# Kernel optimization log

Hardware: AMD Instinct MI355X
Metric: run time of the kernel (lower is better)

## Reference

```python
import jax, jax.numpy as jnp
import numpy as np

N, E = 50000, 800000
D_IN, HID, HEADS, D_OUT = 128, 32, 4, 40
NEG_SLOPE = 0.2
BN_EPS = 1e-5


def gat_conv(x, src, dst, W, a_src, a_dst, b, heads, ch):
    """PyG-style GATConv (eval mode, self-loops already appended to src/dst)."""
    n = x.shape[0]
    h = (x @ W).reshape(n, heads, ch)                      # [N,H,C]
    al_src = jnp.einsum('nhc,hc->nh', h, a_src)            # [N,H]
    al_dst = jnp.einsum('nhc,hc->nh', h, a_dst)
    e = jax.nn.leaky_relu(al_src[src] + al_dst[dst], NEG_SLOPE)  # [Etot,H]
    # segment softmax over incoming edges of each dst node
    e_max = jax.ops.segment_max(e, dst, num_segments=n)
    e = jnp.exp(e - e_max[dst])
    denom = jax.ops.segment_sum(e, dst, num_segments=n)
    alpha = e / (denom[dst] + 1e-16)                        # [Etot,H]
    msg = h[src] * alpha[:, :, None]                        # [Etot,H,C]
    out = jax.ops.segment_sum(msg, dst, num_segments=n)     # [N,H,C]
    return out.reshape(n, heads * ch) + b


def bn_eval(x, g, b, m, v):
    return (x - m) * jax.lax.rsqrt(v + BN_EPS) * g + b


def setup_inputs() -> dict:
    key = jax.random.key(0)
    ks = jax.random.split(key, 24)
    p = lambda k, s: jax.random.normal(k, s, jnp.float32) * 0.1
    inp = {
        'x': jax.random.normal(ks[0], (N, D_IN), jnp.float32),
        'edge_index': jax.random.randint(ks[1], (2, E), 0, N),
        'W1': p(ks[2], (D_IN, HEADS * HID)),
        'a_src1': p(ks[3], (HEADS, HID)), 'a_dst1': p(ks[4], (HEADS, HID)),
        'b1': jnp.zeros((HEADS * HID,), jnp.float32),
        'W2': p(ks[5], (HEADS * HID, HEADS * HID)),
        'a_src2': p(ks[6], (HEADS, HID)), 'a_dst2': p(ks[7], (HEADS, HID)),
        'b2': jnp.zeros((HEADS * HID,), jnp.float32),
        'W3': p(ks[8], (HEADS * HID, D_OUT)),
        'a_src3': p(ks[9], (1, D_OUT)), 'a_dst3': p(ks[10], (1, D_OUT)),
        'b3': jnp.zeros((D_OUT,), jnp.float32),
        'bn1_g': jnp.ones((HEADS * HID,), jnp.float32),
        'bn1_b': jnp.zeros((HEADS * HID,), jnp.float32),
        'bn1_m': p(ks[11], (HEADS * HID,)),
        'bn1_v': jax.random.uniform(ks[12], (HEADS * HID,), jnp.float32) + 0.5,
        'bn2_g': jnp.ones((HEADS * HID,), jnp.float32),
        'bn2_b': jnp.zeros((HEADS * HID,), jnp.float32),
        'bn2_m': p(ks[13], (HEADS * HID,)),
        'bn2_v': jax.random.uniform(ks[14], (HEADS * HID,), jnp.float32) + 0.5,
    }
    return inp


def reference(x, edge_index, W1, a_src1, a_dst1, b1, W2, a_src2, a_dst2, b2,
              W3, a_src3, a_dst3, b3, bn1_g, bn1_b, bn1_m, bn1_v,
              bn2_g, bn2_b, bn2_m, bn2_v):
    n = x.shape[0]
    loop = jnp.arange(n, dtype=edge_index.dtype)
    src = jnp.concatenate([edge_index[0], loop])   # add self loops (PyG default)
    dst = jnp.concatenate([edge_index[1], loop])

    h = gat_conv(x, src, dst, W1, a_src1, a_dst1, b1, HEADS, HID)
    h = jax.nn.relu(h)
    h = bn_eval(h, bn1_g, bn1_b, bn1_m, bn1_v)      # dropout = identity (eval)

    h = gat_conv(h, src, dst, W2, a_src2, a_dst2, b2, HEADS, HID)
    h = jax.nn.relu(h)
    h = bn_eval(h, bn2_g, bn2_b, bn2_m, bn2_v)

    h = gat_conv(h, src, dst, W3, a_src3, a_dst3, b3, 1, D_OUT)
    return jax.nn.log_softmax(h, axis=1)
```

## Files before the change

### kernel.cpp

```cpp
#include <hip/hip_runtime.h>
#include <hip/hip_bf16.h>
#include <math.h>

using bf16 = __hip_bfloat16;
using frag8 = __attribute__((ext_vector_type(8))) short;
using f32x4 = __attribute__((ext_vector_type(4))) float;

#define LEAKY 0.2f
#define BN_EPS 1e-5f
#define NEGBIG -1e30f

__device__ __forceinline__ float lrelu(float z){ return z > 0.f ? z : LEAKY * z; }
__device__ __forceinline__ float bflo(unsigned u){ return __uint_as_float(u << 16); }
__device__ __forceinline__ float bfhi(unsigned u){ return __uint_as_float(u & 0xffff0000u); }
__device__ __forceinline__ unsigned pk(float a, float b){
  unsigned ua = __float_as_uint(a), ub = __float_as_uint(b);
  ua += 0x7fffu + ((ua >> 16) & 1u);
  ub += 0x7fffu + ((ub >> 16) & 1u);
  return (ua >> 16) | (ub & 0xffff0000u);
}
__device__ __forceinline__ float ldf(const void* p, size_t i, int isbf){
  if (isbf) return (float)((const bf16*)p)[i];
  return ((const float*)p)[i];
}

union U4F8 { uint4 u; frag8 f; };

__device__ __forceinline__ frag8 load_a_pairs(const unsigned* __restrict__ X2, int node, int k0){
  U4F8 v; v.u = *((const uint4*)(X2 + (size_t)node*64 + (k0 >> 1))); return v.f;
}
__device__ __forceinline__ frag8 load_a_f32(const float* __restrict__ X, int node, int k0){
  float4 q0 = *((const float4*)(X + (size_t)node*128 + k0));
  float4 q1 = *((const float4*)(X + (size_t)node*128 + k0 + 4));
  U4F8 v; v.u = make_uint4(pk(q0.x,q0.y), pk(q0.z,q0.w), pk(q1.x,q1.y), pk(q1.z,q1.w));
  return v.f;
}

__global__ void init_detect(int* head, const unsigned short* __restrict__ w1bits,
                            int* flag, int n){
  int g = blockIdx.x*256 + threadIdx.x;
  if (g < n) head[g] = -1;
  if (blockIdx.x == 0){
    __shared__ int cntr;
    if (threadIdx.x == 0) cntr = 0;
    __syncthreads();
    unsigned u = w1bits[threadIdx.x * 2];
    int e = (u >> 7) & 0xff;
    atomicAdd(&cntr, (e >= 64 && e <= 140) ? 1 : 0);
    __syncthreads();
    if (threadIdx.x == 0) *flag = (cntr >= 160) ? 1 : 0;
  }
}

__global__ void chain_build(const int* __restrict__ dst, int* head, int* next,
                            int e, int n){
  int g = blockIdx.x*256 + threadIdx.x;
  if (g < e){
    int d = dst[g];
    next[g] = ((unsigned)d < (unsigned)n) ? atomicExch(&head[d], g) : -1;
  }
}

__global__ void chain_count(const int* __restrict__ head, const int* __restrict__ next,
                            int* cnt, int* total, int n){
  int g = blockIdx.x*256 + threadIdx.x;
  if (g == 0) *total = 0;
  if (g >= n) return;
  int c = 0;
  for (int e = head[g]; e != -1; e = next[e]) ++c;
  cnt[g] = c;
}

__global__ void csr_scan(const int* __restrict__ cnt, int* start, int* total, int n){
  __shared__ int s[256];
  __shared__ int base_s;
  int t = threadIdx.x;
  int g = blockIdx.x*256 + t;
  int v = (g < n) ? cnt[g] : 0;
  s[t] = v;
  __syncthreads();
  for (int off = 1; off < 256; off <<= 1){
    int x = (t >= off) ? s[t-off] : 0;
    __syncthreads();
    s[t] += x;
    __syncthreads();
  }
  if (t == 255) base_s = atomicAdd(total, s[255]);
  __syncthreads();
  if (g < n) start[g] = base_s + s[t] - v;
}

__global__ void chain_fill(const int* __restrict__ head, const int* __restrict__ next,
                           const int* __restrict__ src, const int* __restrict__ start,
                           int* col, int n){
  int g = blockIdx.x*256 + threadIdx.x;
  if (g >= n) return;
  int p = start[g];
  for (int e = head[g]; e != -1; e = next[e])
    col[p++] = src[e];
}

__global__ __launch_bounds__(256) void gemm_al_mfma(
    const void* __restrict__ X, int xkind,
    const void* __restrict__ W, const void* __restrict__ Wsrc, const void* __restrict__ Wdst,
    const int* __restrict__ flagp,
    unsigned* __restrict__ H2, float* __restrict__ AL, float* __restrict__ AD,
    int n, int ntiles)
{
  __shared__ unsigned short WT[128*136];
  const int isbf = *flagp;
  const int t = threadIdx.x;
  if (isbf){
    const unsigned short* W16 = (const unsigned short*)W;
    for (int idx = t; idx < 16384; idx += 256){
      int k = idx >> 7, nn = idx & 127;
      WT[nn*136 + k] = W16[idx];
    }
  } else {
    const float* Wf = (const float*)W;
    for (int idx = t; idx < 16384; idx += 256){
      int k = idx >> 7, nn = idx & 127;
      WT[nn*136 + k] = (unsigned short)(pk(Wf[idx], 0.f) & 0xffffu);
    }
  }
  __syncthreads();
  const int w = t >> 6;
  const int lane = t & 63;
  const int m = lane & 15, quad = lane >> 4;

  frag8 bf[4][2];
  #pragma unroll
  for (int s = 0; s < 4; ++s)
    #pragma unroll
    for (int ct = 0; ct < 2; ++ct){
      int colc = w*32 + ct*16 + m;
      int k0 = s*32 + quad*8;
      U4F8 v; v.u = *((const uint4*)&WT[colc*136 + k0]);
      bf[s][ct] = v.f;
    }
  float avv[2], dvv[2];
  #pragma unroll
  for (int ct = 0; ct < 2; ++ct){
    int colc = w*32 + ct*16 + m;
    avv[ct] = ldf(Wsrc, colc, isbf);
    dvv[ct] = ldf(Wdst, colc, isbf);
  }
  const bool pairs = (xkind == 1) || isbf;

  for (int tile = blockIdx.x; tile < ntiles; tile += gridDim.x){
    const int mb = tile*16;
    int nodeA = mb + m; if (nodeA >= n) nodeA = n - 1;
    frag8 af[4];
    #pragma unroll
    for (int s = 0; s < 4; ++s){
      int k0 = s*32 + quad*8;
      af[s] = pairs ? load_a_pairs((const unsigned*)X, nodeA, k0)
                    : load_a_f32((const float*)X, nodeA, k0);
    }
    f32x4 acc0 = {0.f,0.f,0.f,0.f}, acc1 = {0.f,0.f,0.f,0.f};
    #pragma unroll
    for (int s = 0; s < 4; ++s){
      acc0 = __builtin_amdgcn_mfma_f32_16x16x32_bf16(af[s], bf[s][0], acc0, 0,0,0);
      acc1 = __builtin_amdgcn_mfma_f32_16x16x32_bf16(af[s], bf[s][1], acc1, 0,0,0);
    }
    #pragma unroll
    for (int r = 0; r < 4; ++r){
      int g = mb + quad*4 + r;
      float v0 = acc0[r], v1 = acc1[r];
      unsigned u0 = pk(v0, __shfl_xor(v0, 1));
      unsigned u1 = pk(v1, __shfl_xor(v1, 1));
      bool ok = g < n;
      if (((lane & 1) == 0) && ok){
        H2[(size_t)g*64 + w*16 + (m >> 1)]     = u0;
        H2[(size_t)g*64 + w*16 + 8 + (m >> 1)] = u1;
      }
      float s1 = v0*avv[0] + v1*avv[1];
      float s2 = v0*dvv[0] + v1*dvv[1];
      s1 += __shfl_xor(s1,1); s1 += __shfl_xor(s1,2); s1 += __shfl_xor(s1,4); s1 += __shfl_xor(s1,8);
      s2 += __shfl_xor(s2,1); s2 += __shfl_xor(s2,2); s2 += __shfl_xor(s2,4); s2 += __shfl_xor(s2,8);
      if (m == 0 && ok){ AL[g*4 + w] = s1; AD[g*4 + w] = s2; }
    }
  }
}

__global__ __launch_bounds__(256) void gemm3_mfma(
    const unsigned* __restrict__ X2, const void* __restrict__ W,
    const void* __restrict__ Wsrc, const void* __restrict__ Wdst,
    const int* __restrict__ flagp,
    unsigned* __restrict__ H3, float* __restrict__ AL, float* __restrict__ AD,
    int n, int ntiles)
{
  __shared__ unsigned short WT[48*136];
  const int isbf = *flagp;
  const int t = threadIdx.x;
  for (int idx = t; idx < 128*64; idx += 256){
    int c = idx & 63, k = idx >> 6;
    if (c < 48){
      unsigned short v = 0;
      if (c < 40){
        if (isbf) v = ((const unsigned short*)W)[k*40 + c];
        else      v = (unsigned short)(pk(((const float*)W)[k*40 + c], 0.f) & 0xffffu);
      }
      WT[c*136 + k] = v;
    }
  }
  __syncthreads();
  const int w = t >> 6;
  const int lane = t & 63;
  const int m = lane & 15, quad = lane >> 4;

  frag8 bf[4][3];
  float avv[3], dvv[3];
  #pragma unroll
  for (int ct = 0; ct < 3; ++ct){
    int colc = ct*16 + m;
    #pragma unroll
    for (int s = 0; s < 4; ++s){
      int k0 = s*32 + quad*8;
      U4F8 v; v.u = *((const uint4*)&WT[colc*136 + k0]);
      bf[s][ct] = v.f;
    }
    avv[ct] = (colc < 40) ? ldf(Wsrc, colc, isbf) : 0.f;
    dvv[ct] = (colc < 40) ? ldf(Wdst, colc, isbf) : 0.f;
  }

  for (int tg = blockIdx.x; tg*4 < ntiles; tg += gridDim.x){
    const int tile = tg*4 + w;
    if (tile >= ntiles) continue;
    const int mb = tile*16;
    int nodeA = mb + m; if (nodeA >= n) nodeA = n - 1;
    frag8 af[4];
    #pragma unroll
    for (int s = 0; s < 4; ++s)
      af[s] = load_a_pairs(X2, nodeA, s*32 + quad*8);
    f32x4 acc[3];
    #pragma unroll
    for (int ct = 0; ct < 3; ++ct) acc[ct] = (f32x4){0.f,0.f,0.f,0.f};
    #pragma unroll
    for (int s = 0; s < 4; ++s){
      acc[0] = __builtin_amdgcn_mfma_f32_16x16x32_bf16(af[s], bf[s][0], acc[0], 0,0,0);
      acc[1] = __builtin_amdgcn_mfma_f32_16x16x32_bf16(af[s], bf[s][1], acc[1], 0,0,0);
      acc[2] = __builtin_amdgcn_mfma_f32_16x16x32_bf16(af[s], bf[s][2], acc[2], 0,0,0);
    }
    #pragma unroll
    for (int r = 0; r < 4; ++r){
      int g = mb + quad*4 + r;
      bool ok = g < n;
      float ps = 0.f, pd = 0.f;
      #pragma unroll
      for (int ct = 0; ct < 3; ++ct){
        float v = acc[ct][r];
        ps += v*avv[ct]; pd += v*dvv[ct];
        unsigned u = pk(v, __shfl_xor(v, 1));
        bool stok = ((lane & 1) == 0) && ok && (ct < 2 || m < 8);
        if (stok) H3[(size_t)g*20 + ct*8 + (m >> 1)] = u;
      }
      ps += __shfl_xor(ps,1); ps += __shfl_xor(ps,2); ps += __shfl_xor(ps,4); ps += __shfl_xor(ps,8);
      pd += __shfl_xor(pd,1); pd += __shfl_xor(pd,2); pd += __shfl_xor(pd,4); pd += __shfl_xor(pd,8);
      if (m == 0 && ok){ AL[g] = ps; AD[g] = pd; }
    }
  }
}

__global__ __launch_bounds__(256) void agg4(
    const unsigned* __restrict__ H2,
    const float* __restrict__ ALf, const float* __restrict__ ADf,
    const int* __restrict__ cnt, const int* __restrict__ start, const int* __restrict__ col,
    const void* __restrict__ bias, const void* __restrict__ bng, const void* __restrict__ bnb,
    const void* __restrict__ bnm,  const void* __restrict__ bnv,
    const int* __restrict__ flagp,
    unsigned* __restrict__ Hout, int n)
{
  const int isbf = *flagp;
  const int wave = threadIdx.x >> 6;
  const int lane = threadIdx.x & 63;
  const int node = blockIdx.x*4 + wave;
  if (node >= n) return;
  const int head = lane >> 4;
  const float ad = ADf[node*4 + head];
  const int base = start[node], deg = cnt[node];

  float accL, accH, l;
  {
    float e = __expf(lrelu(ALf[node*4 + head] + ad));
    unsigned h = H2[(size_t)node*64 + lane];
    l = e; accL = e * bflo(h); accH = e * bfhi(h);
  }

  int i = 0;
  for (; i + 8 <= deg; i += 8){
    int sv[8]; float av[8]; unsigned hv[8];
    #pragma unroll
    for (int u = 0; u < 8; ++u){
      int s = col[base + i + u];
      sv[u] = ((unsigned)s < (unsigned)n) ? s : 0;
    }
    #pragma unroll
    for (int u = 0; u < 8; ++u) av[u] = ALf[sv[u]*4 + head];
    #pragma unroll
    for (int u = 0; u < 8; ++u) hv[u] = H2[(size_t)sv[u]*64 + lane];
    #pragma unroll
    for (int u = 0; u < 8; ++u){
      float e = __expf(lrelu(av[u] + ad));
      l    += e;
      accL += e * bflo(hv[u]);
      accH += e * bfhi(hv[u]);
    }
  }
  for (; i < deg; ++i){
    int s = col[base + i];
    if ((unsigned)s >= (unsigned)n) s = 0;
    float a = ALf[s*4 + head];
    unsigned h = H2[(size_t)s*64 + lane];
    float e = __expf(lrelu(a + ad));
    l += e; accL += e * bflo(h); accH += e * bfhi(h);
  }

  const float rl = 1.f / l;
  const int c0 = 2*lane, c1 = c0 + 1;
  float v0 = fmaxf(accL*rl + ldf(bias,c0,isbf), 0.f);
  v0 = (v0 - ldf(bnm,c0,isbf)) * rsqrtf(ldf(bnv,c0,isbf) + BN_EPS) * ldf(bng,c0,isbf) + ldf(bnb,c0,isbf);
  float v1 = fmaxf(accH*rl + ldf(bias,c1,isbf), 0.f);
  v1 = (v1 - ldf(bnm,c1,isbf)) * rsqrtf(ldf(bnv,c1,isbf) + BN_EPS) * ldf(bng,c1,isbf) + ldf(bnb,c1,isbf);
  Hout[(size_t)node*64 + lane] = pk(v0, v1);
}

__global__ __launch_bounds__(256) void agg1(
    const unsigned* __restrict__ H3,
    const float* __restrict__ AL, const float* __restrict__ AD,
    const int* __restrict__ cnt, const int* __restrict__ start, const int* __restrict__ col,
    const void* __restrict__ b3, const int* __restrict__ flagp,
    void* __restrict__ out, int n)
{
  const int isbf = *flagp;
  const int wave = threadIdx.x >> 6;
  const int lane = threadIdx.x & 63;
  const int node = blockIdx.x*4 + wave;
  if (node >= n) return;
  const float ad = AD[node];
  const bool act = lane < 20;
  const int base = start[node], deg = cnt[node];

  float accL, accH, l;
  {
    float e = __expf(lrelu(AL[node] + ad));
    unsigned h = act ? H3[(size_t)node*20 + lane] : 0u;
    l = e; accL = e * bflo(h); accH = e * bfhi(h);
  }

  int i = 0;
  for (; i + 8 <= deg; i += 8){
    int sv[8]; float av[8]; unsigned hv[8];
    #pragma unroll
    for (int u = 0; u < 8; ++u){
      int s = col[base + i + u];
      sv[u] = ((unsigned)s < (unsigned)n) ? s : 0;
    }
    #pragma unroll
    for (int u = 0; u < 8; ++u) av[u] = AL[sv[u]];
    #pragma unroll
    for (int u = 0; u < 8; ++u) hv[u] = act ? H3[(size_t)sv[u]*20 + lane] : 0u;
    #pragma unroll
    for (int u = 0; u < 8; ++u){
      float e = __expf(lrelu(av[u] + ad));
      l    += e;
      accL += e * bflo(hv[u]);
      accH += e * bfhi(hv[u]);
    }
  }
  for (; i < deg; ++i){
    int s = col[base + i];
    if ((unsigned)s >= (unsigned)n) s = 0;
    float a = AL[s];
    unsigned h = act ? H3[(size_t)s*20 + lane] : 0u;
    float e = __expf(lrelu(a + ad));
    l += e; accL += e * bflo(h); accH += e * bfhi(h);
  }

  const float rl = 1.f / l;
  const int c0 = 2*lane;
  float z0 = act ? (accL*rl + ldf(b3, c0,     isbf)) : NEGBIG;
  float z1 = act ? (accH*rl + ldf(b3, c0 + 1, isbf)) : NEGBIG;
  float mx = fmaxf(z0, z1);
  #pragma unroll
  for (int off = 1; off < 64; off <<= 1) mx = fmaxf(mx, __shfl_xor(mx, off));
  float p = act ? (__expf(z0 - mx) + __expf(z1 - mx)) : 0.f;
  float sum = p;
  #pragma unroll
  for (int off = 1; off < 64; off <<= 1) sum += __shfl_xor(sum, off);
  if (act){
    float lg = __logf(sum);
    float r0 = z0 - mx - lg, r1 = z1 - mx - lg;
    if (isbf) ((unsigned*)out)[(size_t)node*20 + lane] = pk(r0, r1);
    else      ((float2*)out)[(size_t)node*20 + lane] = make_float2(r0, r1);
  }
}

extern "C" void kernel_launch(void* const* d_in, const int* in_sizes, int n_in,
                              void* d_out, int out_size, void* d_ws, size_t ws_size,
                              hipStream_t stream)
{
  (void)n_in; (void)out_size; (void)ws_size;
  const void* x    = d_in[0];
  const int*  ei   = (const int*)d_in[1];
  const void* W1   = d_in[2];
  const void* as1  = d_in[3];
  const void* ad1  = d_in[4];
  const void* b1   = d_in[5];
  const void* W2   = d_in[6];
  const void* as2  = d_in[7];
  const void* ad2  = d_in[8];
  const void* b2   = d_in[9];
  const void* W3   = d_in[10];
  const void* as3  = d_in[11];
  const void* ad3  = d_in[12];
  const void* b3   = d_in[13];
  const void* bn1g = d_in[14];
  const void* bn1b = d_in[15];
  const void* bn1m = d_in[16];
  const void* bn1v = d_in[17];
  const void* bn2g = d_in[18];
  const void* bn2b = d_in[19];
  const void* bn2m = d_in[20];
  const void* bn2v = d_in[21];

  const int N  = in_sizes[0] / 128;
  const int E  = in_sizes[1] / 2;
  const int ntiles = (N + 15) / 16;

  char* w = (char*)d_ws;
  size_t off = 0;
  auto alloc = [&](size_t bytes)->char*{
    char* p = w + off; off = (off + bytes + 255) & ~(size_t)255; return p;
  };
  unsigned* H2A = (unsigned*)alloc((size_t)N*64*4);
  unsigned* H2B = (unsigned*)alloc((size_t)N*64*4);
  unsigned* H3p = (unsigned*)alloc((size_t)N*20*4);
  float* AL   = (float*)alloc((size_t)N*4*4);
  float* AD   = (float*)alloc((size_t)N*4*4);
  int*   headp = (int*)alloc((size_t)N*4);
  int*   nextp = (int*)alloc((size_t)E*4);
  int*   cnt   = (int*)alloc((size_t)N*4);
  int*   start = (int*)alloc((size_t)N*4);
  int*   col   = (int*)alloc((size_t)E*4);
  int*   flag  = (int*)alloc(256);
  int*   total = (int*)alloc(256);

  const int* srcp = ei;
  const int* dstp = ei + E;

  const int nb256 = (N + 255)/256, eb256 = (E + 255)/256;
  const int bb = (N + 3)/4;
  int g1 = ntiles < 625 ? ntiles : 625;
  int g3 = (ntiles + 3)/4; if (g3 > 400) g3 = 400;

  init_detect<<<nb256,256,0,stream>>>(headp, (const unsigned short*)W1, flag, N);
  chain_build<<<eb256,256,0,stream>>>(dstp, headp, nextp, E, N);
  chain_count<<<nb256,256,0,stream>>>(headp, nextp, cnt, total, N);
  csr_scan  <<<nb256,256,0,stream>>>(cnt, start, total, N);
  chain_fill<<<nb256,256,0,stream>>>(headp, nextp, srcp, start, col, N);

  gemm_al_mfma<<<g1,256,0,stream>>>(x, 0, W1, as1, ad1, flag, H2A, AL, AD, N, ntiles);
  agg4<<<bb,256,0,stream>>>(H2A, AL, AD, cnt, start, col,
                            b1, bn1g, bn1b, bn1m, bn1v, flag, H2B, N);
  gemm_al_mfma<<<g1,256,0,stream>>>(H2B, 1, W2, as2, ad2, flag, H2A, AL, AD, N, ntiles);
  agg4<<<bb,256,0,stream>>>(H2A, AL, AD, cnt, start, col,
                            b2, bn2g, bn2b, bn2m, bn2v, flag, H2B, N);
  gemm3_mfma<<<g3,256,0,stream>>>(H2B, W3, as3, ad3, flag, H3p, AL, AD, N, ntiles);
  agg1<<<bb,256,0,stream>>>(H3p, AL, AD, cnt, start, col, b3, flag, d_out, N);
}
```

Measured before the change: 384.4 us.

## Replace linked-list CSR build with histogram plus bucketed two-pass sort

Swaps the atomicExch linked-list chain construction, with its serial pointer-chasing count and fill passes, for a degree histogram, a coarse bucket sort of (src,dst) pairs by dst range through shared memory, and a per-bucket scatter into CSR. This is meant to remove the dependent random loads of chain traversal and to localise the scatter writes so they stay cache-friendly. The cost is two extra kernels, an 8-byte-per-edge staging buffer, and atomics on the per-node positions. It also turns leaky-relu into an fmax.

```diff
diff --git a/kernel.cpp b/kernel.cpp
--- a/kernel.cpp
+++ b/kernel.cpp
@@ -9,8 +9,9 @@
 #define LEAKY 0.2f
 #define BN_EPS 1e-5f
 #define NEGBIG -1e30f
-
-__device__ __forceinline__ float lrelu(float z){ return z > 0.f ? z : LEAKY * z; }
+#define BSHIFT 9
+
+__device__ __forceinline__ float lrelu(float z){ return fmaxf(z, LEAKY * z); }
 __device__ __forceinline__ float bflo(unsigned u){ return __uint_as_float(u << 16); }
 __device__ __forceinline__ float bfhi(unsigned u){ return __uint_as_float(u & 0xffff0000u); }
 __device__ __forceinline__ unsigned pk(float a, float b){
@@ -36,10 +37,12 @@
   return v.f;
 }
 
-__global__ void init_detect(int* head, const unsigned short* __restrict__ w1bits,
-                            int* flag, int n){
+__global__ void init_detect(int* cnt, int* bcnt, const unsigned short* __restrict__ w1bits,
+                            int* flag, int* total, int n){
   int g = blockIdx.x*256 + threadIdx.x;
-  if (g < n) head[g] = -1;
+  if (g < n) cnt[g] = 0;
+  if (g < 256) bcnt[g] = 0;
+  if (g == 0) *total = 0;
   if (blockIdx.x == 0){
     __shared__ int cntr;
     if (threadIdx.x == 0) cntr = 0;
@@ -52,26 +55,27 @@
   }
 }
 
-__global__ void chain_build(const int* __restrict__ dst, int* head, int* next,
-                            int e, int n){
-  int g = blockIdx.x*256 + threadIdx.x;
-  if (g < e){
-    int d = dst[g];
-    next[g] = ((unsigned)d < (unsigned)n) ? atomicExch(&head[d], g) : -1;
-  }
-}
-
-__global__ void chain_count(const int* __restrict__ head, const int* __restrict__ next,
-                            int* cnt, int* total, int n){
-  int g = blockIdx.x*256 + threadIdx.x;
-  if (g == 0) *total = 0;
-  if (g >= n) return;
-  int c = 0;
-  for (int e = head[g]; e != -1; e = next[e]) ++c;
-  cnt[g] = c;
-}
-
-__global__ void csr_scan(const int* __restrict__ cnt, int* start, int* total, int n){
+__global__ __launch_bounds__(256) void hist(const int* __restrict__ dst, int* cnt,
+                                            int* bcnt, int e, int n){
+  __shared__ int lb[256];
+  const int t = threadIdx.x;
+  lb[t] = 0;
+  __syncthreads();
+  const int c0 = blockIdx.x*4096;
+  const int lim = min(4096, e - c0);
+  for (int i = t; i < lim; i += 256){
+    int d = dst[c0 + i];
+    if ((unsigned)d < (unsigned)n){
+      atomicAdd(&cnt[d], 1);
+      atomicAdd(&lb[min(d >> BSHIFT, 255)], 1);
+    }
+  }
+  __syncthreads();
+  if (lb[t]) atomicAdd(&bcnt[t], lb[t]);
+}
+
+__global__ void csr_scan(const int* __restrict__ cnt, int* start, int* pos,
+                         int* total, int n){
   __shared__ int s[256];
   __shared__ int base_s;
   int t = threadIdx.x;
@@ -87,17 +91,96 @@
   }
   if (t == 255) base_s = atomicAdd(total, s[255]);
   __syncthreads();
-  if (g < n) start[g] = base_s + s[t] - v;
-}
-
-__global__ void chain_fill(const int* __restrict__ head, const int* __restrict__ next,
-                           const int* __restrict__ src, const int* __restrict__ start,
-                           int* col, int n){
-  int g = blockIdx.x*256 + threadIdx.x;
-  if (g >= n) return;
-  int p = start[g];
-  for (int e = head[g]; e != -1; e = next[e])
-    col[p++] = src[e];
+  if (g < n){
+    int st = base_s + s[t] - v;
+    start[g] = st;
+    pos[g] = st;
+  }
+}
+
+__global__ void bscan(const int* __restrict__ bcnt, int* bstart, int* bpos){
+  __shared__ int s[256];
+  int t = threadIdx.x;
+  int v = bcnt[t];
+  s[t] = v;
+  __syncthreads();
+  for (int off = 1; off < 256; off <<= 1){
+    int x = (t >= off) ? s[t-off] : 0;
+    __syncthreads();
+    s[t] += x;
+    __syncthreads();
+  }
+  int st = s[t] - v;
+  bstart[t] = st;
+  bpos[t] = st;
+}
+
+__global__ __launch_bounds__(256) void bsort(const int* __restrict__ src,
+                                             const int* __restrict__ dst,
+                                             int* bpos, int2* __restrict__ ebuf,
+                                             int e, int n){
+  __shared__ int lh[256], lo[256], gb[256];
+  __shared__ int tot_s;
+  __shared__ int2 buf[4096];
+  const int t = threadIdx.x;
+  const int c0 = blockIdx.x*4096;
+  if (c0 >= e) return;
+  const int lim = min(4096, e - c0);
+  lh[t] = 0;
+  __syncthreads();
+  int2 ev[16]; int bk[16];
+  #pragma unroll
+  for (int j = 0; j < 16; ++j){
+    const int i = j*256 + t;
+    const bool valid = i < lim;
+    int s = 0, d = 0;
+    if (valid){ s = src[c0 + i]; d = dst[c0 + i]; }
+    ev[j] = make_int2(s, d);
+    bk[j] = (valid && (unsigned)d < (unsigned)n) ? min(d >> BSHIFT, 255) : -1;
+    if (bk[j] >= 0) atomicAdd(&lh[bk[j]], 1);
+  }
+  __syncthreads();
+  const int v = lh[t];
+  lo[t] = v;
+  __syncthreads();
+  for (int off = 1; off < 256; off <<= 1){
+    int x = (t >= off) ? lo[t-off] : 0;
+    __syncthreads();
+    lo[t] += x;
+    __syncthreads();
+  }
+  if (t == 255) tot_s = lo[255];
+  lo[t] -= v;
+  if (v) gb[t] = atomicAdd(&bpos[t], v);
+  lh[t] = 0;
+  __syncthreads();
+  #pragma unroll
+  for (int j = 0; j < 16; ++j){
+    if (bk[j] >= 0){
+      int r = atomicAdd(&lh[bk[j]], 1);
+      buf[lo[bk[j]] + r] = ev[j];
+    }
+  }
+  __syncthreads();
+  const int tot = tot_s;
+  for (int i = t; i < tot; i += 256){
+    int2 sd = buf[i];
+    int b = min(sd.y >> BSHIFT, 255);
+    ebuf[gb[b] + (i - lo[b])] = sd;
+  }
+}
+
+__global__ __launch_bounds__(512) void cscat(const int2* __restrict__ ebuf,
+                                             const int* __restrict__ bstart,
+                                             const int* __restrict__ bpos,
+                                             int* pos, int* __restrict__ col){
+  const int b = blockIdx.x;
+  const int s1 = bpos[b];
+  for (int i = bstart[b] + threadIdx.x; i < s1; i += 512){
+    int2 sd = ebuf[i];
+    int p = atomicAdd(&pos[sd.y], 1);
+    col[p] = sd.x;
+  }
 }
 
 __global__ __launch_bounds__(256) void gemm_al_mfma(
@@ -438,27 +521,32 @@
   unsigned* H3p = (unsigned*)alloc((size_t)N*20*4);
   float* AL   = (float*)alloc((size_t)N*4*4);
   float* AD   = (float*)alloc((size_t)N*4*4);
-  int*   headp = (int*)alloc((size_t)N*4);
-  int*   nextp = (int*)alloc((size_t)E*4);
   int*   cnt   = (int*)alloc((size_t)N*4);
   int*   start = (int*)alloc((size_t)N*4);
+  int*   pos   = (int*)alloc((size_t)N*4);
   int*   col   = (int*)alloc((size_t)E*4);
+  int2*  ebuf  = (int2*)alloc((size_t)E*8);
+  int*   bcnt  = (int*)alloc(1024);
+  int*   bstart= (int*)alloc(1024);
+  int*   bpos  = (int*)alloc(1024);
   int*   flag  = (int*)alloc(256);
   int*   total = (int*)alloc(256);
 
   const int* srcp = ei;
   const int* dstp = ei + E;
 
-  const int nb256 = (N + 255)/256, eb256 = (E + 255)/256;
+  const int nb256 = (N + 255)/256;
+  const int nbCH = (E + 4095)/4096;
   const int bb = (N + 3)/4;
   int g1 = ntiles < 625 ? ntiles : 625;
   int g3 = (ntiles + 3)/4; if (g3 > 400) g3 = 400;
 
-  init_detect<<<nb256,256,0,stream>>>(headp, (const unsigned short*)W1, flag, N);
-  chain_build<<<eb256,256,0,stream>>>(dstp, headp, nextp, E, N);
-  chain_count<<<nb256,256,0,stream>>>(headp, nextp, cnt, total, N);
-  csr_scan  <<<nb256,256,0,stream>>>(cnt, start, total, N);
-  chain_fill<<<nb256,256,0,stream>>>(headp, nextp, srcp, start, col, N);
+  init_detect<<<nb256,256,0,stream>>>(cnt, bcnt, (const unsigned short*)W1, flag, total, N);
+  hist<<<nbCH,256,0,stream>>>(dstp, cnt, bcnt, E, N);
+  csr_scan<<<nb256,256,0,stream>>>(cnt, start, pos, total, N);
+  bscan<<<1,256,0,stream>>>(bcnt, bstart, bpos);
+  bsort<<<nbCH,256,0,stream>>>(srcp, dstp, bpos, ebuf, E, N);
+  cscat<<<256,512,0,stream>>>(ebuf, bstart, bpos, pos, col);
 
   gemm_al_mfma<<<g1,256,0,stream>>>(x, 0, W1, as1, ad1, flag, H2A, AL, AD, N, ntiles);
   agg4<<<bb,256,0,stream>>>(H2A, AL, AD, cnt, start, col,
```

Measured after the change: 397.0 us. +3.3%, slower.

## Count degrees atomically in chain build and share edge exps across lanes

Applied to the files above, without the earlier changes.

Removes the chain_count kernel: chain_build now increments per-node degree counters with atomicAdd, and init_detect zeroes the counters and the total. The cost removed is a serial pointer-chasing walk of every linked list. In agg4 and agg1, each lane now computes one exp for one (edge, head) pair and the values are broadcast with __shfl, instead of every lane redundantly gathering AL and computing eight exps. It also switches lrelu to fmax and the accumulations to explicit fma, at the price of extra atomics and shuffle traffic.

```diff
diff --git a/kernel.cpp b/kernel.cpp
--- a/kernel.cpp
+++ b/kernel.cpp
@@ -10,7 +10,7 @@
 #define BN_EPS 1e-5f
 #define NEGBIG -1e30f
 
-__device__ __forceinline__ float lrelu(float z){ return z > 0.f ? z : LEAKY * z; }
+__device__ __forceinline__ float lrelu(float z){ return fmaxf(z, LEAKY * z); }
 __device__ __forceinline__ float bflo(unsigned u){ return __uint_as_float(u << 16); }
 __device__ __forceinline__ float bfhi(unsigned u){ return __uint_as_float(u & 0xffff0000u); }
 __device__ __forceinline__ unsigned pk(float a, float b){
@@ -36,10 +36,11 @@
   return v.f;
 }
 
-__global__ void init_detect(int* head, const unsigned short* __restrict__ w1bits,
-                            int* flag, int n){
+__global__ void init_detect(int* head, int* cnt, const unsigned short* __restrict__ w1bits,
+                            int* flag, int* total, int n){
   int g = blockIdx.x*256 + threadIdx.x;
-  if (g < n) head[g] = -1;
+  if (g < n){ head[g] = -1; cnt[g] = 0; }
+  if (g == 0) *total = 0;
   if (blockIdx.x == 0){
     __shared__ int cntr;
     if (threadIdx.x == 0) cntr = 0;
@@ -53,22 +54,17 @@
 }
 
 __global__ void chain_build(const int* __restrict__ dst, int* head, int* next,
-                            int e, int n){
+                            int* cnt, int e, int n){
   int g = blockIdx.x*256 + threadIdx.x;
   if (g < e){
     int d = dst[g];
-    next[g] = ((unsigned)d < (unsigned)n) ? atomicExch(&head[d], g) : -1;
-  }
-}
-
-__global__ void chain_count(const int* __restrict__ head, const int* __restrict__ next,
-                            int* cnt, int* total, int n){
-  int g = blockIdx.x*256 + threadIdx.x;
-  if (g == 0) *total = 0;
-  if (g >= n) return;
-  int c = 0;
-  for (int e = head[g]; e != -1; e = next[e]) ++c;
-  cnt[g] = c;
+    if ((unsigned)d < (unsigned)n){
+      next[g] = atomicExch(&head[d], g);
+      atomicAdd(&cnt[d], 1);
+    } else {
+      next[g] = -1;
+    }
+  }
 }
 
 __global__ void csr_scan(const int* __restrict__ cnt, int* start, int* total, int n){
@@ -278,6 +274,9 @@
   if (node >= n) return;
   const int head = lane >> 4;
   const float ad = ADf[node*4 + head];
+  const int eu = (lane >> 2) & 7;
+  const int eh = lane & 3;
+  const float ade = ADf[node*4 + eh];
   const int base = start[node], deg = cnt[node];
 
   float accL, accH, l;
@@ -289,22 +288,22 @@
 
   int i = 0;
   for (; i + 8 <= deg; i += 8){
-    int sv[8]; float av[8]; unsigned hv[8];
+    int sv[8]; unsigned hv[8];
     #pragma unroll
     for (int u = 0; u < 8; ++u){
       int s = col[base + i + u];
       sv[u] = ((unsigned)s < (unsigned)n) ? s : 0;
     }
-    #pragma unroll
-    for (int u = 0; u < 8; ++u) av[u] = ALf[sv[u]*4 + head];
+    float ave = ALf[sv[eu]*4 + eh];
     #pragma unroll
     for (int u = 0; u < 8; ++u) hv[u] = H2[(size_t)sv[u]*64 + lane];
+    float ew = __expf(lrelu(ave + ade));
     #pragma unroll
     for (int u = 0; u < 8; ++u){
-      float e = __expf(lrelu(av[u] + ad));
+      float e = __shfl(ew, (u << 2) + head);
       l    += e;
-      accL += e * bflo(hv[u]);
-      accH += e * bfhi(hv[u]);
+      accL = fmaf(e, bflo(hv[u]), accL);
+      accH = fmaf(e, bfhi(hv[u]), accH);
     }
   }
   for (; i < deg; ++i){
@@ -339,6 +338,7 @@
   if (node >= n) return;
   const float ad = AD[node];
   const bool act = lane < 20;
+  const int eu = lane & 7;
   const int base = start[node], deg = cnt[node];
 
   float accL, accH, l;
@@ -350,22 +350,22 @@
 
   int i = 0;
   for (; i + 8 <= deg; i += 8){
-    int sv[8]; float av[8]; unsigned hv[8];
+    int sv[8]; unsigned hv[8];
     #pragma unroll
     for (int u = 0; u < 8; ++u){
       int s = col[base + i + u];
       sv[u] = ((unsigned)s < (unsigned)n) ? s : 0;
     }
-    #pragma unroll
-    for (int u = 0; u < 8; ++u) av[u] = AL[sv[u]];
+    float ave = AL[sv[eu]];
     #pragma unroll
     for (int u = 0; u < 8; ++u) hv[u] = act ? H3[(size_t)sv[u]*20 + lane] : 0u;
+    float ew = __expf(lrelu(ave + ad));
     #pragma unroll
     for (int u = 0; u < 8; ++u){
-      float e = __expf(lrelu(av[u] + ad));
+      float e = __shfl(ew, u);
       l    += e;
-      accL += e * bflo(hv[u]);
-      accH += e * bfhi(hv[u]);
+      accL = fmaf(e, bflo(hv[u]), accL);
+      accH = fmaf(e, bfhi(hv[u]), accH);
     }
   }
   for (; i < deg; ++i){
@@ -454,9 +454,8 @@
   int g1 = ntiles < 625 ? ntiles : 625;
   int g3 = (ntiles + 3)/4; if (g3 > 400) g3 = 400;
 
-  init_detect<<<nb256,256,0,stream>>>(headp, (const unsigned short*)W1, flag, N);
-  chain_build<<<eb256,256,0,stream>>>(dstp, headp, nextp, E, N);
-  chain_count<<<nb256,256,0,stream>>>(headp, nextp, cnt, total, N);
+  init_detect<<<nb256,256,0,stream>>>(headp, cnt, (const unsigned short*)W1, flag, total, N);
+  chain_build<<<eb256,256,0,stream>>>(dstp, headp, nextp, cnt, E, N);
   csr_scan  <<<nb256,256,0,stream>>>(cnt, start, total, N);
   chain_fill<<<nb256,256,0,stream>>>(headp, nextp, srcp, start, col, N);
 
```

Result: slower. 404.3 us (+5.2%).
